# Performance work log

Hardware: AMD Instinct MI355X
Metric: run time of the kernel (lower is better)

The kernel has to match this reference:

```python
import jax, jax.numpy as jnp
import numpy as np


def setup_inputs() -> dict:
    key = jax.random.key(0)
    k1, k2, k3, k4 = jax.random.split(key, 4)
    B, T, E, H = 4, 2048, 1024, 16
    hs = E // H
    x = jax.random.normal(k1, (B, T, E), dtype=jnp.float32)
    # per-head projection weights (nn.Linear bias=False, stored as [H, E, head_size])
    s = 1.0 / np.sqrt(E)
    Wq = jax.random.uniform(k2, (H, E, hs), dtype=jnp.float32, minval=-s, maxval=s)
    Wk = jax.random.uniform(k3, (H, E, hs), dtype=jnp.float32, minval=-s, maxval=s)
    Wv = jax.random.uniform(k4, (H, E, hs), dtype=jnp.float32, minval=-s, maxval=s)
    return {"x": x, "Wq": Wq, "Wk": Wk, "Wv": Wv}


def reference(x, Wq, Wk, Wv):
    # x: [B, T, E]; Wq/Wk/Wv: [H, E, hs]
    B, T, E = x.shape
    H = Wq.shape[0]
    q = jnp.einsum('bte,hed->bhtd', x, Wq)
    k = jnp.einsum('bte,hed->bhtd', x, Wk)
    v = jnp.einsum('bte,hed->bhtd', x, Wv)
    scores = jnp.einsum('bhtd,bhsd->bhts', q, k)
    # causal mask applied before scaling (matches original; -inf unaffected by scale)
    causal = jnp.tril(jnp.ones((T, T), dtype=bool))
    scores = jnp.where(causal, scores, -jnp.inf)
    # NOTE: original scales by sqrt(embed_size), not sqrt(head_size)
    scores = scores / jnp.sqrt(jnp.asarray(E, dtype=scores.dtype))
    w = jax.nn.softmax(scores, axis=-1)
    # dropout: eval mode (identity)
    out = jnp.einsum('bhts,bhsd->bhtd', w, v)  # [B,H,T,hs]
    out = jnp.transpose(out, (0, 2, 1, 3)).reshape(B, T, -1)  # concat heads
    return out
```

## Files before the change

### kernel.cpp

```cpp
#include <hip/hip_runtime.h>
#include <cstdint>
#include <cmath>


typedef __attribute__((ext_vector_type(8))) __bf16 bf16x8;
typedef __attribute__((ext_vector_type(4))) __bf16 bf16x4;
typedef __attribute__((ext_vector_type(4))) float f32x4;
typedef __attribute__((ext_vector_type(16))) float f32x16;

#define B_ 4
#define T_ 2048
#define E_ 1024
#define H_ 16
#define HS_ 64

__device__ __forceinline__ f32x4 mfma16(bf16x8 a, bf16x8 b, f32x4 c) {
  return __builtin_amdgcn_mfma_f32_16x16x32_bf16(a, b, c, 0, 0, 0);
}
__device__ __forceinline__ f32x16 mfma32(bf16x8 a, bf16x8 b, f32x16 c) {
  return __builtin_amdgcn_mfma_f32_32x32x16_bf16(a, b, c, 0, 0, 0);
}

__device__ __forceinline__ void gload_lds16(const void* g, void* l) {
  __builtin_amdgcn_global_load_lds(
      (const __attribute__((address_space(1))) unsigned int*)g,
      (__attribute__((address_space(3))) unsigned int*)l,
      16, 0, 0);
}

__device__ __forceinline__ unsigned cvt_pk_bf16(float lo, float hi) {
  unsigned r;
  asm("v_cvt_pk_bf16_f32 %0, %1, %2" : "=v"(r) : "v"(lo), "v"(hi));
  return r;
}
__device__ __forceinline__ void pl32swap(unsigned& a, unsigned& b) {
  asm("v_permlane32_swap_b32 %0, %1" : "+v"(a), "+v"(b));
}
__device__ __forceinline__ void barrier_asm() {
  asm volatile("s_barrier" ::: "memory");
}

__global__ __launch_bounds__(256) void cvt_x_kernel(const float* __restrict__ x,
                                                    __bf16* __restrict__ xb) {
  int i = (blockIdx.x * 256 + threadIdx.x) * 4;
  float4 v = *(const float4*)(x + i);
  bf16x4 o;
  o[0] = (__bf16)v.x; o[1] = (__bf16)v.y; o[2] = (__bf16)v.z; o[3] = (__bf16)v.w;
  *(bf16x4*)(xb + i) = o;
}

__global__ __launch_bounds__(256) void cvt_w_kernel(const float* __restrict__ Wq,
                                                    const float* __restrict__ Wk,
                                                    const float* __restrict__ Wv,
                                                    __bf16* __restrict__ wt) {
  __shared__ float tile[64][65];
  const int e0 = blockIdx.x * 64;
  const int h = blockIdx.y;
  const int qkv = blockIdx.z;
  const int t = threadIdx.x;
  const float* W = (qkv == 0) ? Wq : (qkv == 1) ? Wk : Wv;
#pragma unroll
  for (int j = 0; j < 4; ++j) {
    int idx = j * 256 + t;
    int d4 = idx & 15, e = idx >> 4;
    float4 v = *(const float4*)&W[((size_t)(h * 1024 + e0 + e)) * 64 + d4 * 4];
    tile[d4 * 4 + 0][e] = v.x;
    tile[d4 * 4 + 1][e] = v.y;
    tile[d4 * 4 + 2][e] = v.z;
    tile[d4 * 4 + 3][e] = v.w;
  }
  __syncthreads();
#pragma unroll
  for (int j = 0; j < 2; ++j) {
    int idx = j * 256 + t;
    int e8 = idx & 7, d = idx >> 3;
    bf16x8 o;
#pragma unroll
    for (int i = 0; i < 8; ++i) o[i] = (__bf16)tile[d][e8 * 8 + i];
    *(bf16x8*)&wt[((size_t)qkv << 20) + (size_t)(h * 64 + d) * 1024 + e0 + e8 * 8] = o;
  }
}

__global__ __launch_bounds__(256) void qkv_gemm_kernel(
    const __bf16* __restrict__ Xb, const __bf16* __restrict__ Wt,
    __bf16* __restrict__ Qb, __bf16* __restrict__ Kb, __bf16* __restrict__ Vt) {
  __shared__ __bf16 As[3][128 * 32];
  __shared__ __bf16 Bs[3][128 * 32];
  const int qkv = blockIdx.z;
  const int m0 = blockIdx.x * 128;
  const int n0 = blockIdx.y * 128;
  const int t = threadIdx.x;
  const int lane = t & 63;
  const int w = t >> 6, wr = w >> 1, wc = w & 1;
  const int g = lane >> 4, c = lane & 15;

  const __bf16* wsrc = Wt + ((size_t)qkv << 20);
  f32x4 acc[4][4] = {};

  const int srow = t >> 2;
  const int cs8 = (((t & 3) ^ (srow & 3)) << 3);
  const __bf16* gA0 = Xb + (size_t)(m0 + srow) * 1024 + cs8;
  const __bf16* gA1 = Xb + (size_t)(m0 + 64 + srow) * 1024 + cs8;
  const __bf16* gB0 = wsrc + (size_t)(n0 + srow) * 1024 + cs8;
  const __bf16* gB1 = wsrc + (size_t)(n0 + 64 + srow) * 1024 + cs8;

  auto stage = [&](int s, int slot) {
    const int ko = s * 32;
    gload_lds16(gA0 + ko, &As[slot][t * 8]);
    gload_lds16(gA1 + ko, &As[slot][2048 + t * 8]);
    gload_lds16(gB0 + ko, &Bs[slot][t * 8]);
    gload_lds16(gB1 + ko, &Bs[slot][2048 + t * 8]);
  };

  stage(0, 0);
  stage(1, 1);

  const int gx = (g ^ (c & 3)) << 3;
  int slot = 0;

#pragma unroll 1
  for (int kt = 0; kt < 32; ++kt) {
    if (kt < 31) {
      asm volatile("s_waitcnt vmcnt(4)" ::: "memory");
    } else {
      asm volatile("s_waitcnt vmcnt(0)" ::: "memory");
    }
    __builtin_amdgcn_sched_barrier(0);
    barrier_asm();
    if (kt + 2 < 32) {
      int ns = slot + 2; if (ns >= 3) ns -= 3;
      stage(kt + 2, ns);
    }

    const __bf16* Ab = &As[slot][0];
    const __bf16* Bb = &Bs[slot][0];
    bf16x8 af[4], bfr[4];
#pragma unroll
    for (int mi = 0; mi < 4; ++mi)
      af[mi] = *(const bf16x8*)&Ab[(wr * 64 + mi * 16 + c) * 32 + gx];
#pragma unroll
    for (int ni = 0; ni < 4; ++ni)
      bfr[ni] = *(const bf16x8*)&Bb[(wc * 64 + ni * 16 + c) * 32 + gx];
    __builtin_amdgcn_s_setprio(1);
#pragma unroll
    for (int mi = 0; mi < 4; ++mi)
#pragma unroll
      for (int ni = 0; ni < 4; ++ni)
        acc[mi][ni] = mfma16(af[mi], bfr[ni], acc[mi][ni]);
    __builtin_amdgcn_s_setprio(0);
    __builtin_amdgcn_sched_barrier(0);
    slot = (slot == 2) ? 0 : slot + 1;
  }

  const int mbase = m0 + wr * 64 + g * 4;
  const int nbase = n0 + wc * 64 + c;
  if (qkv < 2) {
    __bf16* dst = (qkv == 0) ? Qb : Kb;
#pragma unroll
    for (int mi = 0; mi < 4; ++mi) {
#pragma unroll
      for (int ni = 0; ni < 4; ++ni) {
        int n = nbase + ni * 16;
        int h = n >> 6, d = n & 63;
#pragma unroll
        for (int r = 0; r < 4; ++r) {
          int m = mbase + mi * 16 + r;
          int b = m >> 11, tt = m & 2047;
          dst[(((size_t)b * H_ + h) * T_ + tt) * HS_ + d] = (__bf16)acc[mi][ni][r];
        }
      }
    }
  } else {
#pragma unroll
    for (int mi = 0; mi < 4; ++mi) {
      int m = mbase + mi * 16;
      int b = m >> 11, tt = m & 2047;
#pragma unroll
      for (int ni = 0; ni < 4; ++ni) {
        int n = nbase + ni * 16;
        int h = n >> 6, d = n & 63;
        bf16x4 pk;
        pk[0] = (__bf16)acc[mi][ni][0];
        pk[1] = (__bf16)acc[mi][ni][1];
        pk[2] = (__bf16)acc[mi][ni][2];
        pk[3] = (__bf16)acc[mi][ni][3];
        *(bf16x4*)&Vt[(((size_t)b * H_ + h) * HS_ + d) * T_ + tt] = pk;
      }
    }
  }
}

__global__ __launch_bounds__(512) void attn_kernel(
    const __bf16* __restrict__ Qb, const __bf16* __restrict__ Kb,
    const __bf16* __restrict__ Vt, float* __restrict__ out) {
  __shared__ __bf16 Ks[3][64 * 64];
  __shared__ __bf16 Vs[3][64 * 64];

  const int j = blockIdx.x;
  const int g8 = j >> 6;
  const int qt = (g8 < 4) ? (7 - g8) : (g8 - 4);
  const int bh = j & 63;
  const int b = bh >> 4, hh = bh & 15;
  const int t = threadIdx.x;
  const int lane = t & 63, w = t >> 6;
  const int lr = lane & 31, h = lane >> 5;

  const __bf16* Qg = Qb + (size_t)bh * T_ * HS_;
  const __bf16* Kg = Kb + (size_t)bh * T_ * HS_;
  const __bf16* Vg = Vt + (size_t)bh * HS_ * T_;

  const int srow = t >> 3;
  const int scb = ((t & 7) << 4) ^ ((srow & 7) << 4);
  const int kxor = (lr & 7) << 4;

  auto stageKV = [&](int s, int slot) {
    gload_lds16((const char*)Kg + (size_t)(s * 64 + srow) * 128 + scb,
                (char*)&Ks[slot][0] + t * 16);
    gload_lds16((const char*)Vg + (size_t)srow * 4096 + s * 128 + scb,
                (char*)&Vs[slot][0] + t * 16);
  };

  const float C2 = 0.04508422f;

  const int qbase = qt * 256;
  const int NT = (qt + 1) * 4;
  const int tqg = qbase + w * 32 + lr;

  const __bf16* Qrow = Qg + (size_t)tqg * 64;
  bf16x8 qf0 = *(const bf16x8*)(Qrow + h * 8);
  bf16x8 qf1 = *(const bf16x8*)(Qrow + 16 + h * 8);
  bf16x8 qf2 = *(const bf16x8*)(Qrow + 32 + h * 8);
  bf16x8 qf3 = *(const bf16x8*)(Qrow + 48 + h * 8);

  f32x16 o0 = {}, o1 = {};
  float m_run = -INFINITY, l_run = 0.f;

  stageKV(0, 0);
  stageKV(1, 1);
  int slot = 0;

#pragma unroll 1
  for (int kt = 0; kt < NT; ++kt) {
    const int kbase = kt * 64;
    if (kt + 1 < NT) {
      asm volatile("s_waitcnt vmcnt(2)" ::: "memory");
    } else {
      asm volatile("s_waitcnt vmcnt(0)" ::: "memory");
    }
    __builtin_amdgcn_sched_barrier(0);
    barrier_asm();
    if (kt + 2 < NT) {
      int ns = slot + 2; if (ns >= 3) ns -= 3;
      stageKV(kt + 2, ns);
    }

    if (kbase <= qbase + w * 32 + 31) {
      const char* KsB = (const char*)&Ks[slot][0];
      const char* VsB = (const char*)&Vs[slot][0];

      f32x16 s0 = {}, s1 = {};
      __builtin_amdgcn_s_setprio(1);
#pragma unroll
      for (int ds = 0; ds < 4; ++ds) {
        bf16x8 k0 = *(const bf16x8*)(KsB + ((lr * 128 + ds * 32 + h * 16) ^ kxor));
        bf16x8 k1 = *(const bf16x8*)(KsB + (((lr + 32) * 128 + ds * 32 + h * 16) ^ kxor));
        bf16x8 qd = (ds == 0) ? qf0 : (ds == 1) ? qf1 : (ds == 2) ? qf2 : qf3;
        s0 = mfma32(k0, qd, s0);
        s1 = mfma32(k1, qd, s1);
      }
      __builtin_amdgcn_s_setprio(0);

      if (kbase + 63 > qbase + w * 32) {
#pragma unroll
        for (int r = 0; r < 16; ++r) {
          int tk0 = kbase + (r & 3) + 8 * (r >> 2) + 4 * h;
          if (tk0 > tqg) s0[r] = -INFINITY;
          if (tk0 + 32 > tqg) s1[r] = -INFINITY;
        }
      }

      float mx = s0[0];
#pragma unroll
      for (int r = 1; r < 16; ++r) mx = fmaxf(mx, s0[r]);
#pragma unroll
      for (int r = 0; r < 16; ++r) mx = fmaxf(mx, s1[r]);
      mx = fmaxf(mx, __shfl_xor(mx, 32));
      if (!__all(mx - m_run <= 256.f)) {
        float mn = fmaxf(m_run, mx);
        float fac = __builtin_amdgcn_exp2f((m_run - mn) * C2);
        l_run *= fac;
#pragma unroll
        for (int r = 0; r < 16; ++r) { o0[r] *= fac; o1[r] *= fac; }
        m_run = mn;
      }
      float sum = 0.f;
#pragma unroll
      for (int r = 0; r < 16; ++r) {
        s0[r] = __builtin_amdgcn_exp2f((s0[r] - m_run) * C2);
        s1[r] = __builtin_amdgcn_exp2f((s1[r] - m_run) * C2);
        sum += s0[r] + s1[r];
      }
      sum += __shfl_xor(sum, 32);
      l_run += sum;

      __builtin_amdgcn_s_setprio(1);
#pragma unroll
      for (int blk = 0; blk < 4; ++blk) {
        f32x16& sv = (blk < 2) ? s0 : s1;
        const int off = (blk & 1) * 8;
        unsigned u0 = cvt_pk_bf16(sv[off + 0], sv[off + 1]);
        unsigned u1 = cvt_pk_bf16(sv[off + 2], sv[off + 3]);
        unsigned u2 = cvt_pk_bf16(sv[off + 4], sv[off + 5]);
        unsigned u3 = cvt_pk_bf16(sv[off + 6], sv[off + 7]);
        pl32swap(u0, u2);
        pl32swap(u1, u3);
        union { unsigned u[4]; bf16x8 v; } pb;
        pb.u[0] = u0; pb.u[1] = u1; pb.u[2] = u2; pb.u[3] = u3;
        bf16x8 v0 = *(const bf16x8*)(VsB + ((lr * 128 + blk * 32 + h * 16) ^ kxor));
        bf16x8 v1 = *(const bf16x8*)(VsB + (((lr + 32) * 128 + blk * 32 + h * 16) ^ kxor));
        o0 = mfma32(v0, pb.v, o0);
        o1 = mfma32(v1, pb.v, o1);
      }
      __builtin_amdgcn_s_setprio(0);
    }
    slot = (slot == 2) ? 0 : slot + 1;
  }

  const float inv_l = 1.0f / l_run;
  float* orow = out + ((size_t)b * T_ + tqg) * E_ + hh * 64;
#pragma unroll
  for (int d0i = 0; d0i < 2; ++d0i) {
#pragma unroll
    for (int qd = 0; qd < 4; ++qd) {
      float4 v;
      const f32x16& ac = d0i ? o1 : o0;
      v.x = ac[qd * 4 + 0] * inv_l;
      v.y = ac[qd * 4 + 1] * inv_l;
      v.z = ac[qd * 4 + 2] * inv_l;
      v.w = ac[qd * 4 + 3] * inv_l;
      *(float4*)(orow + d0i * 32 + qd * 8 + 4 * h) = v;
    }
  }
}

extern "C" void kernel_launch(void* const* d_in, const int* in_sizes, int n_in,
                              void* d_out, int out_size, void* d_ws, size_t ws_size,
                              hipStream_t stream) {
  const float* x = (const float*)d_in[0];
  const float* Wq = (const float*)d_in[1];
  const float* Wk = (const float*)d_in[2];
  const float* Wv = (const float*)d_in[3];
  float* out = (float*)d_out;

  char* ws = (char*)d_ws;
  __bf16* Xb = (__bf16*)ws;
  __bf16* Wt = (__bf16*)(ws + (16u << 20));
  __bf16* Qb = (__bf16*)(ws + (22u << 20));
  __bf16* Kb = (__bf16*)(ws + (38u << 20));
  __bf16* Vt = (__bf16*)(ws + (54u << 20));

  cvt_x_kernel<<<8192, 256, 0, stream>>>(x, Xb);
  cvt_w_kernel<<<dim3(16, 16, 3), 256, 0, stream>>>(Wq, Wk, Wv, Wt);
  qkv_gemm_kernel<<<dim3(64, 8, 3), 256, 0, stream>>>(Xb, Wt, Qb, Kb, Vt);
  attn_kernel<<<dim3(512), 512, 0, stream>>>(Qb, Kb, Vt, out);
}
```

Measured before the change: 211.9 us.

## Drop LDS staging in attention; load K/V directly from global per wave

The attention kernel no longer stages K/V tiles through a triple-buffered LDS ring with barriers. Each wave now reads its K and V fragments straight from global memory (relying on L2/L1 for reuse) and runs its own causal loop length. Blocks shrink from 512 to 256 threads and cover 128 query rows, so the grid grows to 1024 with a new four-group ordering of query tiles for load balance. This removes the barrier and LDS costs and per-block idle waves, but each wave now fetches K/V on its own, raising global/L2 traffic, and no software prefetch is left to hide load latency.

```diff
diff --git a/kernel.cpp b/kernel.cpp
--- a/kernel.cpp
+++ b/kernel.cpp
@@ -190,16 +190,14 @@
   }
 }
 
-__global__ __launch_bounds__(512) void attn_kernel(
+__global__ __launch_bounds__(256) void attn_kernel(
     const __bf16* __restrict__ Qb, const __bf16* __restrict__ Kb,
     const __bf16* __restrict__ Vt, float* __restrict__ out) {
-  __shared__ __bf16 Ks[3][64 * 64];
-  __shared__ __bf16 Vs[3][64 * 64];
-
   const int j = blockIdx.x;
-  const int g8 = j >> 6;
-  const int qt = (g8 < 4) ? (7 - g8) : (g8 - 4);
   const int bh = j & 63;
+  const int qs = j >> 6;
+  const int gq = qs >> 2, iq = qs & 3;
+  const int qt = (gq == 0) ? 15 - iq : (gq == 1) ? iq : (gq == 2) ? 11 - iq : 4 + iq;
   const int b = bh >> 4, hh = bh & 15;
   const int t = threadIdx.x;
   const int lane = t & 63, w = t >> 6;
@@ -209,121 +207,98 @@
   const __bf16* Kg = Kb + (size_t)bh * T_ * HS_;
   const __bf16* Vg = Vt + (size_t)bh * HS_ * T_;
 
-  const int srow = t >> 3;
-  const int scb = ((t & 7) << 4) ^ ((srow & 7) << 4);
-  const int kxor = (lr & 7) << 4;
-
-  auto stageKV = [&](int s, int slot) {
-    gload_lds16((const char*)Kg + (size_t)(s * 64 + srow) * 128 + scb,
-                (char*)&Ks[slot][0] + t * 16);
-    gload_lds16((const char*)Vg + (size_t)srow * 4096 + s * 128 + scb,
-                (char*)&Vs[slot][0] + t * 16);
-  };
-
   const float C2 = 0.04508422f;
 
-  const int qbase = qt * 256;
-  const int NT = (qt + 1) * 4;
-  const int tqg = qbase + w * 32 + lr;
+  const int wrow = qt * 128 + w * 32;
+  const int tqg = wrow + lr;
+  const int NTw = wrow / 64 + 1;
 
   const __bf16* Qrow = Qg + (size_t)tqg * 64;
-  bf16x8 qf0 = *(const bf16x8*)(Qrow + h * 8);
-  bf16x8 qf1 = *(const bf16x8*)(Qrow + 16 + h * 8);
-  bf16x8 qf2 = *(const bf16x8*)(Qrow + 32 + h * 8);
-  bf16x8 qf3 = *(const bf16x8*)(Qrow + 48 + h * 8);
+  bf16x8 qf[4];
+#pragma unroll
+  for (int ds = 0; ds < 4; ++ds)
+    qf[ds] = *(const bf16x8*)(Qrow + ds * 16 + h * 8);
 
   f32x16 o0 = {}, o1 = {};
   float m_run = -INFINITY, l_run = 0.f;
 
-  stageKV(0, 0);
-  stageKV(1, 1);
-  int slot = 0;
-
 #pragma unroll 1
-  for (int kt = 0; kt < NT; ++kt) {
+  for (int kt = 0; kt < NTw; ++kt) {
     const int kbase = kt * 64;
-    if (kt + 1 < NT) {
-      asm volatile("s_waitcnt vmcnt(2)" ::: "memory");
-    } else {
-      asm volatile("s_waitcnt vmcnt(0)" ::: "memory");
-    }
-    __builtin_amdgcn_sched_barrier(0);
-    barrier_asm();
-    if (kt + 2 < NT) {
-      int ns = slot + 2; if (ns >= 3) ns -= 3;
-      stageKV(kt + 2, ns);
-    }
-
-    if (kbase <= qbase + w * 32 + 31) {
-      const char* KsB = (const char*)&Ks[slot][0];
-      const char* VsB = (const char*)&Vs[slot][0];
-
-      f32x16 s0 = {}, s1 = {};
-      __builtin_amdgcn_s_setprio(1);
-#pragma unroll
-      for (int ds = 0; ds < 4; ++ds) {
-        bf16x8 k0 = *(const bf16x8*)(KsB + ((lr * 128 + ds * 32 + h * 16) ^ kxor));
-        bf16x8 k1 = *(const bf16x8*)(KsB + (((lr + 32) * 128 + ds * 32 + h * 16) ^ kxor));
-        bf16x8 qd = (ds == 0) ? qf0 : (ds == 1) ? qf1 : (ds == 2) ? qf2 : qf3;
-        s0 = mfma32(k0, qd, s0);
-        s1 = mfma32(k1, qd, s1);
+
+    const __bf16* Kr0 = Kg + (size_t)(kbase + lr) * 64 + h * 8;
+    const __bf16* Kr1 = Kr0 + 32 * 64;
+    bf16x8 kf0[4], kf1[4];
+#pragma unroll
+    for (int ds = 0; ds < 4; ++ds) {
+      kf0[ds] = *(const bf16x8*)(Kr0 + ds * 16);
+      kf1[ds] = *(const bf16x8*)(Kr1 + ds * 16);
+    }
+
+    f32x16 s0 = {}, s1 = {};
+#pragma unroll
+    for (int ds = 0; ds < 4; ++ds) {
+      s0 = mfma32(kf0[ds], qf[ds], s0);
+      s1 = mfma32(kf1[ds], qf[ds], s1);
+    }
+
+    const __bf16* Vr0 = Vg + (size_t)lr * (size_t)T_ + kbase + h * 8;
+    const __bf16* Vr1 = Vr0 + (size_t)32 * T_;
+    bf16x8 vf0[4], vf1[4];
+#pragma unroll
+    for (int blk = 0; blk < 4; ++blk) {
+      vf0[blk] = *(const bf16x8*)(Vr0 + blk * 16);
+      vf1[blk] = *(const bf16x8*)(Vr1 + blk * 16);
+    }
+
+    if (kbase + 63 > wrow) {
+#pragma unroll
+      for (int r = 0; r < 16; ++r) {
+        int tk0 = kbase + (r & 3) + 8 * (r >> 2) + 4 * h;
+        if (tk0 > tqg) s0[r] = -INFINITY;
+        if (tk0 + 32 > tqg) s1[r] = -INFINITY;
       }
-      __builtin_amdgcn_s_setprio(0);
-
-      if (kbase + 63 > qbase + w * 32) {
-#pragma unroll
-        for (int r = 0; r < 16; ++r) {
-          int tk0 = kbase + (r & 3) + 8 * (r >> 2) + 4 * h;
-          if (tk0 > tqg) s0[r] = -INFINITY;
-          if (tk0 + 32 > tqg) s1[r] = -INFINITY;
-        }
-      }
-
-      float mx = s0[0];
-#pragma unroll
-      for (int r = 1; r < 16; ++r) mx = fmaxf(mx, s0[r]);
-#pragma unroll
-      for (int r = 0; r < 16; ++r) mx = fmaxf(mx, s1[r]);
-      mx = fmaxf(mx, __shfl_xor(mx, 32));
-      if (!__all(mx - m_run <= 256.f)) {
-        float mn = fmaxf(m_run, mx);
-        float fac = __builtin_amdgcn_exp2f((m_run - mn) * C2);
-        l_run *= fac;
-#pragma unroll
-        for (int r = 0; r < 16; ++r) { o0[r] *= fac; o1[r] *= fac; }
-        m_run = mn;
-      }
-      float sum = 0.f;
-#pragma unroll
-      for (int r = 0; r < 16; ++r) {
-        s0[r] = __builtin_amdgcn_exp2f((s0[r] - m_run) * C2);
-        s1[r] = __builtin_amdgcn_exp2f((s1[r] - m_run) * C2);
-        sum += s0[r] + s1[r];
-      }
-      sum += __shfl_xor(sum, 32);
-      l_run += sum;
-
-      __builtin_amdgcn_s_setprio(1);
-#pragma unroll
-      for (int blk = 0; blk < 4; ++blk) {
-        f32x16& sv = (blk < 2) ? s0 : s1;
-        const int off = (blk & 1) * 8;
-        unsigned u0 = cvt_pk_bf16(sv[off + 0], sv[off + 1]);
-        unsigned u1 = cvt_pk_bf16(sv[off + 2], sv[off + 3]);
-        unsigned u2 = cvt_pk_bf16(sv[off + 4], sv[off + 5]);
-        unsigned u3 = cvt_pk_bf16(sv[off + 6], sv[off + 7]);
-        pl32swap(u0, u2);
-        pl32swap(u1, u3);
-        union { unsigned u[4]; bf16x8 v; } pb;
-        pb.u[0] = u0; pb.u[1] = u1; pb.u[2] = u2; pb.u[3] = u3;
-        bf16x8 v0 = *(const bf16x8*)(VsB + ((lr * 128 + blk * 32 + h * 16) ^ kxor));
-        bf16x8 v1 = *(const bf16x8*)(VsB + (((lr + 32) * 128 + blk * 32 + h * 16) ^ kxor));
-        o0 = mfma32(v0, pb.v, o0);
-        o1 = mfma32(v1, pb.v, o1);
-      }
-      __builtin_amdgcn_s_setprio(0);
-    }
-    slot = (slot == 2) ? 0 : slot + 1;
+    }
+
+    float mx = s0[0];
+#pragma unroll
+    for (int r = 1; r < 16; ++r) mx = fmaxf(mx, s0[r]);
+#pragma unroll
+    for (int r = 0; r < 16; ++r) mx = fmaxf(mx, s1[r]);
+    mx = fmaxf(mx, __shfl_xor(mx, 32));
+    if (!__all(mx - m_run <= 256.f)) {
+      float mn = fmaxf(m_run, mx);
+      float fac = __builtin_amdgcn_exp2f((m_run - mn) * C2);
+      l_run *= fac;
+#pragma unroll
+      for (int r = 0; r < 16; ++r) { o0[r] *= fac; o1[r] *= fac; }
+      m_run = mn;
+    }
+    float sum = 0.f;
+#pragma unroll
+    for (int r = 0; r < 16; ++r) {
+      s0[r] = __builtin_amdgcn_exp2f((s0[r] - m_run) * C2);
+      s1[r] = __builtin_amdgcn_exp2f((s1[r] - m_run) * C2);
+      sum += s0[r] + s1[r];
+    }
+    sum += __shfl_xor(sum, 32);
+    l_run += sum;
+
+#pragma unroll
+    for (int blk = 0; blk < 4; ++blk) {
+      f32x16& sv = (blk < 2) ? s0 : s1;
+      const int off = (blk & 1) * 8;
+      unsigned u0 = cvt_pk_bf16(sv[off + 0], sv[off + 1]);
+      unsigned u1 = cvt_pk_bf16(sv[off + 2], sv[off + 3]);
+      unsigned u2 = cvt_pk_bf16(sv[off + 4], sv[off + 5]);
+      unsigned u3 = cvt_pk_bf16(sv[off + 6], sv[off + 7]);
+      pl32swap(u0, u2);
+      pl32swap(u1, u3);
+      union { unsigned u[4]; bf16x8 v; } pb;
+      pb.u[0] = u0; pb.u[1] = u1; pb.u[2] = u2; pb.u[3] = u3;
+      o0 = mfma32(vf0[blk], pb.v, o0);
+      o1 = mfma32(vf1[blk], pb.v, o1);
+    }
   }
 
   const float inv_l = 1.0f / l_run;
@@ -362,5 +337,5 @@
   cvt_x_kernel<<<8192, 256, 0, stream>>>(x, Xb);
   cvt_w_kernel<<<dim3(16, 16, 3), 256, 0, stream>>>(Wq, Wk, Wv, Wt);
   qkv_gemm_kernel<<<dim3(64, 8, 3), 256, 0, stream>>>(Xb, Wt, Qb, Kb, Vt);
-  attn_kernel<<<dim3(512), 512, 0, stream>>>(Qb, Kb, Vt, out);
-}
+  attn_kernel<<<dim3(1024), 256, 0, stream>>>(Qb, Kb, Vt, out);
+}
```

Measured after the change: 293.1 us. +38.3%, slower.

## Restructure QKV GEMM to 128x256 tiles with 8 waves and K=64 double buffering

Applied to the files above, without the earlier changes.

The QKV projection GEMM moves from 128x128 tiles with 4 waves and a triple-buffered K=32 pipeline to 128x256 tiles with 8 waves, a double-buffered K=64 stage, and a new 8-way XOR swizzle. Within each K tile the A prefetch is split to overlap with the second half of the MFMA work. The intent is more reuse of each loaded X tile across a wider N tile and fewer loop iterations and barriers. In exchange LDS use rises, there are more barriers per iteration, and the grid has half as many blocks, which could lower occupancy.

```diff
diff --git a/kernel.cpp b/kernel.cpp
--- a/kernel.cpp
+++ b/kernel.cpp
@@ -81,79 +81,107 @@
   }
 }
 
-__global__ __launch_bounds__(256) void qkv_gemm_kernel(
+__global__ __launch_bounds__(512) void qkv_gemm_kernel(
     const __bf16* __restrict__ Xb, const __bf16* __restrict__ Wt,
     __bf16* __restrict__ Qb, __bf16* __restrict__ Kb, __bf16* __restrict__ Vt) {
-  __shared__ __bf16 As[3][128 * 32];
-  __shared__ __bf16 Bs[3][128 * 32];
+  __shared__ __bf16 As[2 * 128 * 64];
+  __shared__ __bf16 Bs[2 * 256 * 64];
   const int qkv = blockIdx.z;
   const int m0 = blockIdx.x * 128;
-  const int n0 = blockIdx.y * 128;
+  const int n0 = blockIdx.y * 256;
   const int t = threadIdx.x;
   const int lane = t & 63;
-  const int w = t >> 6, wr = w >> 1, wc = w & 1;
-  const int g = lane >> 4, c = lane & 15;
+  const int wid = t >> 6;
+  const int wm = wid >> 2, wn = wid & 3;
+  const int c = lane & 15, g = lane >> 4;
 
   const __bf16* wsrc = Wt + ((size_t)qkv << 20);
   f32x4 acc[4][4] = {};
 
-  const int srow = t >> 2;
-  const int cs8 = (((t & 3) ^ (srow & 3)) << 3);
-  const __bf16* gA0 = Xb + (size_t)(m0 + srow) * 1024 + cs8;
-  const __bf16* gA1 = Xb + (size_t)(m0 + 64 + srow) * 1024 + cs8;
-  const __bf16* gB0 = wsrc + (size_t)(n0 + srow) * 1024 + cs8;
-  const __bf16* gB1 = wsrc + (size_t)(n0 + 64 + srow) * 1024 + cs8;
-
-  auto stage = [&](int s, int slot) {
-    const int ko = s * 32;
-    gload_lds16(gA0 + ko, &As[slot][t * 8]);
-    gload_lds16(gA1 + ko, &As[slot][2048 + t * 8]);
-    gload_lds16(gB0 + ko, &Bs[slot][t * 8]);
-    gload_lds16(gB1 + ko, &Bs[slot][2048 + t * 8]);
+  const int r0 = t >> 3;
+  const int sl = t & 7;
+  const int swz = ((sl ^ (r0 & 7)) * 8);
+  const __bf16* gA = Xb + (size_t)(m0 + r0) * 1024 + swz;
+  const __bf16* gB = wsrc + (size_t)(n0 + r0) * 1024 + swz;
+
+  auto stageA = [&](int tt, int buf) {
+    const int ko = tt * 64;
+    char* dst = (char*)As + buf * 16384 + t * 16;
+    gload_lds16(gA + ko, dst);
+    gload_lds16(gA + 64 * 1024 + ko, dst + 8192);
   };
-
-  stage(0, 0);
-  stage(1, 1);
-
-  const int gx = (g ^ (c & 3)) << 3;
-  int slot = 0;
+  auto stageB = [&](int tt, int buf) {
+    const int ko = tt * 64;
+    char* dst = (char*)Bs + buf * 32768 + t * 16;
+#pragma unroll
+    for (int q = 0; q < 4; ++q)
+      gload_lds16(gB + q * 64 * 1024 + ko, dst + q * 8192);
+  };
+
+  const int cz = c & 7;
+  const int sw0 = ((0 + g) ^ cz) * 16;
+  const int sw1 = ((4 + g) ^ cz) * 16;
+  const int arow = (wm * 64 + c) * 128;
+  const int brow = (wn * 64 + c) * 128;
+
+  stageB(0, 0);
+  stageA(0, 0);
 
 #pragma unroll 1
-  for (int kt = 0; kt < 32; ++kt) {
-    if (kt < 31) {
+  for (int tt = 0; tt < 16; ++tt) {
+    const int buf = tt & 1;
+    const bool pre = (tt + 1 < 16);
+    const char* AsB = (const char*)As + buf * 16384;
+    const char* BsB = (const char*)Bs + buf * 32768;
+
+    if (pre) {
+      stageB(tt + 1, buf ^ 1);
       asm volatile("s_waitcnt vmcnt(4)" ::: "memory");
     } else {
       asm volatile("s_waitcnt vmcnt(0)" ::: "memory");
     }
-    __builtin_amdgcn_sched_barrier(0);
     barrier_asm();
-    if (kt + 2 < 32) {
-      int ns = slot + 2; if (ns >= 3) ns -= 3;
-      stage(kt + 2, ns);
-    }
-
-    const __bf16* Ab = &As[slot][0];
-    const __bf16* Bb = &Bs[slot][0];
-    bf16x8 af[4], bfr[4];
-#pragma unroll
-    for (int mi = 0; mi < 4; ++mi)
-      af[mi] = *(const bf16x8*)&Ab[(wr * 64 + mi * 16 + c) * 32 + gx];
-#pragma unroll
-    for (int ni = 0; ni < 4; ++ni)
-      bfr[ni] = *(const bf16x8*)&Bb[(wc * 64 + ni * 16 + c) * 32 + gx];
-    __builtin_amdgcn_s_setprio(1);
-#pragma unroll
-    for (int mi = 0; mi < 4; ++mi)
-#pragma unroll
-      for (int ni = 0; ni < 4; ++ni)
-        acc[mi][ni] = mfma16(af[mi], bfr[ni], acc[mi][ni]);
-    __builtin_amdgcn_s_setprio(0);
-    __builtin_amdgcn_sched_barrier(0);
-    slot = (slot == 2) ? 0 : slot + 1;
-  }
-
-  const int mbase = m0 + wr * 64 + g * 4;
-  const int nbase = n0 + wc * 64 + c;
+    {
+      bf16x8 aF[4], bF[4];
+#pragma unroll
+      for (int i = 0; i < 4; ++i)
+        aF[i] = *(const bf16x8*)(AsB + arow + i * 2048 + sw0);
+#pragma unroll
+      for (int jj = 0; jj < 4; ++jj)
+        bF[jj] = *(const bf16x8*)(BsB + brow + jj * 2048 + sw0);
+      __builtin_amdgcn_s_setprio(1);
+#pragma unroll
+      for (int i = 0; i < 4; ++i)
+#pragma unroll
+        for (int jj = 0; jj < 4; ++jj)
+          acc[i][jj] = mfma16(aF[i], bF[jj], acc[i][jj]);
+      __builtin_amdgcn_s_setprio(0);
+    }
+    barrier_asm();
+
+    {
+      bf16x8 aF[4], bF[4];
+#pragma unroll
+      for (int i = 0; i < 4; ++i)
+        aF[i] = *(const bf16x8*)(AsB + arow + i * 2048 + sw1);
+#pragma unroll
+      for (int jj = 0; jj < 4; ++jj)
+        bF[jj] = *(const bf16x8*)(BsB + brow + jj * 2048 + sw1);
+      if (pre) stageA(tt + 1, buf ^ 1);
+      barrier_asm();
+      __builtin_amdgcn_s_setprio(1);
+#pragma unroll
+      for (int i = 0; i < 4; ++i)
+#pragma unroll
+        for (int jj = 0; jj < 4; ++jj)
+          acc[i][jj] = mfma16(aF[i], bF[jj], acc[i][jj]);
+      __builtin_amdgcn_s_setprio(0);
+    }
+    barrier_asm();
+  }
+
+  const int mbase = m0 + wm * 64 + g * 4;
+  const int nbase = n0 + wn * 64 + c;
   if (qkv < 2) {
     __bf16* dst = (qkv == 0) ? Qb : Kb;
 #pragma unroll
@@ -165,8 +193,8 @@
 #pragma unroll
         for (int r = 0; r < 4; ++r) {
           int m = mbase + mi * 16 + r;
-          int b = m >> 11, tt = m & 2047;
-          dst[(((size_t)b * H_ + h) * T_ + tt) * HS_ + d] = (__bf16)acc[mi][ni][r];
+          int b = m >> 11, tt2 = m & 2047;
+          dst[(((size_t)b * H_ + h) * T_ + tt2) * HS_ + d] = (__bf16)acc[mi][ni][r];
         }
       }
     }
@@ -174,7 +202,7 @@
 #pragma unroll
     for (int mi = 0; mi < 4; ++mi) {
       int m = mbase + mi * 16;
-      int b = m >> 11, tt = m & 2047;
+      int b = m >> 11, tt2 = m & 2047;
 #pragma unroll
       for (int ni = 0; ni < 4; ++ni) {
         int n = nbase + ni * 16;
@@ -184,7 +212,7 @@
         pk[1] = (__bf16)acc[mi][ni][1];
         pk[2] = (__bf16)acc[mi][ni][2];
         pk[3] = (__bf16)acc[mi][ni][3];
-        *(bf16x4*)&Vt[(((size_t)b * H_ + h) * HS_ + d) * T_ + tt] = pk;
+        *(bf16x4*)&Vt[(((size_t)b * H_ + h) * HS_ + d) * T_ + tt2] = pk;
       }
     }
   }
@@ -361,6 +389,6 @@
 
   cvt_x_kernel<<<8192, 256, 0, stream>>>(x, Xb);
   cvt_w_kernel<<<dim3(16, 16, 3), 256, 0, stream>>>(Wq, Wk, Wv, Wt);
-  qkv_gemm_kernel<<<dim3(64, 8, 3), 256, 0, stream>>>(Xb, Wt, Qb, Kb, Vt);
+  qkv_gemm_kernel<<<dim3(64, 4, 3), 512, 0, stream>>>(Xb, Wt, Qb, Kb, Vt);
   attn_kernel<<<dim3(512), 512, 0, stream>>>(Qb, Kb, Vt, out);
 }
```

Result: slower. 222.6 us (+5.0%).
